# Kernel optimization log

Hardware: AMD Instinct MI355X
Metric: run time of the kernel (lower is better)

Reference implementation:

```python
import jax, jax.numpy as jnp
import numpy as np

HIDDEN_DIM = 64
MEMORY_SLOTS = 8
SEQ_LEN = 64
VOCAB_SIZE = 64
B = 524288


def setup_inputs() -> dict:
    key = jax.random.key(0)
    k1, k2, k3, k4, k5, k6 = jax.random.split(key, 6)
    seqs = jax.random.randint(k1, (B, SEQ_LEN), 0, VOCAB_SIZE + 2, dtype=jnp.int64 if jax.config.jax_enable_x64 else jnp.int32)
    query_tok = jax.random.randint(k2, (B,), 0, VOCAB_SIZE + 2, dtype=seqs.dtype)
    embed = jax.random.normal(k3, (VOCAB_SIZE + 2, HIDDEN_DIM), dtype=jnp.float32)
    # torch Linear: y = x @ W.T + b
    W1 = jax.random.normal(k4, (HIDDEN_DIM, HIDDEN_DIM * 2), dtype=jnp.float32) * (1.0 / np.sqrt(HIDDEN_DIM * 2))
    b1 = jnp.zeros((HIDDEN_DIM,), dtype=jnp.float32)
    W2 = jax.random.normal(k5, (VOCAB_SIZE, HIDDEN_DIM), dtype=jnp.float32) * (1.0 / np.sqrt(HIDDEN_DIM))
    b2 = jnp.zeros((VOCAB_SIZE,), dtype=jnp.float32)
    return {"seqs": seqs, "query_tok": query_tok, "embed": embed,
            "W1": W1, "b1": b1, "W2": W2, "b2": b2}


def reference(seqs, query_tok, embed, W1, b1, W2, b2):
    # FIFO of capacity MEMORY_SLOTS over tokens t=0..SEQ_LEN-2 keeps exactly the
    # last MEMORY_SLOTS tokens: positions [SEQ_LEN-1-MEMORY_SLOTS, SEQ_LEN-1).
    win = seqs[:, SEQ_LEN - 1 - MEMORY_SLOTS : SEQ_LEN - 1]        # [B, 8]
    mem_summary = embed[win].mean(axis=1)                          # [B, H]
    q_emb = embed[query_tok]                                       # [B, H]
    h = jnp.concatenate([q_emb, mem_summary], axis=-1)             # [B, 2H]
    h = jax.nn.relu(h @ W1.T + b1)                                 # [B, H]
    logits = h @ W2.T + b2                                         # [B, VOCAB]
    return logits
```

## Files before the change

kernel.cpp:

```cpp
#include <hip/hip_runtime.h>

#define HID 64
#define NTOK 66
#define SEQ 64
#define WIN0 55
#define NW 8
#define LDS_STRIDE 72
#define ITERS 8
#define ROWS_PER_ITER 64

typedef _Float16 half8 __attribute__((ext_vector_type(8)));
typedef unsigned short ushort8v __attribute__((ext_vector_type(8)));
typedef float float4v __attribute__((ext_vector_type(4)));

static __device__ __forceinline__ unsigned short f2h(float f) {
    _Float16 h = (_Float16)f;
    union { _Float16 h; unsigned short u; } v; v.h = h;
    return v.u;
}

__global__ void build_tables(const float* __restrict__ embed,
                             const float* __restrict__ W1,
                             const float* __restrict__ b1,
                             unsigned short* __restrict__ tbl) {
    int b = blockIdx.x;
    int tb = b & 1;
    int t  = b >> 1;
    int n  = threadIdx.x;
    float acc = tb ? 0.0f : b1[n];
    const float* er = embed + t * HID;
    const float* wr = W1 + n * (2 * HID) + tb * HID;
#pragma unroll 8
    for (int k = 0; k < HID; ++k) acc += er[k] * wr[k];
    if (tb) acc *= 0.125f;
    tbl[tb * (NTOK * HID) + t * HID + n] = f2h(acc);
}

__global__ __launch_bounds__(256, 3) void fused_forward(
    const int* __restrict__ seqs,
    const int* __restrict__ qtok,
    const float* __restrict__ W2,
    const float* __restrict__ b2,
    const unsigned short* __restrict__ tbl,
    float* __restrict__ out)
{
    __shared__ unsigned short T_lds[2 * NTOK * LDS_STRIDE];

    int tid  = threadIdx.x;
    int wv   = tid >> 6;
    int l    = tid & 63;
    int lrow = l & 15;
    int lg   = l >> 4;
    int lk8  = lg * 8;

    int row0 = blockIdx.x * (ITERS * ROWS_PER_ITER) + wv * 16 + lrow;

    int qA, qB;
    int wA[NW], wB[NW];
    half8  g[9];
    half8  a0, a1;
    float4v acc4[4];

#define LOADT(s, t_) { \
    int row_ = row0 + (t_) * ROWS_PER_ITER; \
    q##s = qtok[row_]; \
    const int* sp_ = seqs + row_ * SEQ + WIN0; \
    _Pragma("unroll") \
    for (int j = 0; j < NW; ++j) w##s[j] = sp_[j]; \
}

#define GATHER_ALL(qq, ww, k0c) { \
    g[8] = *(const half8*)(T_lds + (qq) * LDS_STRIDE + (k0c)); \
    _Pragma("unroll") \
    for (int j = 0; j < NW; ++j) \
        g[j] = *(const half8*)(T_lds + NTOK * LDS_STRIDE + (ww)[j] * LDS_STRIDE + (k0c)); \
}

#define SUM_REISSUE(aout, qq, ww, k0c) { \
    half8 s_ = g[8]; \
    g[8] = *(const half8*)(T_lds + (qq) * LDS_STRIDE + (k0c)); \
    _Pragma("unroll") \
    for (int j = 0; j < NW; ++j) { \
        s_ += g[j]; \
        g[j] = *(const half8*)(T_lds + NTOK * LDS_STRIDE + (ww)[j] * LDS_STRIDE + (k0c)); \
    } \
    half8 z_ = (half8)(_Float16)0; \
    aout = __builtin_elementwise_max(s_, z_); \
}

#define SUM_FINAL(aout) { \
    half8 s_ = g[8]; \
    _Pragma("unroll") \
    for (int j = 0; j < NW; ++j) s_ += g[j]; \
    half8 z_ = (half8)(_Float16)0; \
    aout = __builtin_elementwise_max(s_, z_); \
}

#define MFMA_K0 { \
    _Pragma("unroll") \
    for (int nt = 0; nt < 4; ++nt) \
        acc4[nt] = __builtin_amdgcn_mfma_f32_16x16x32_f16(wfrag[nt][0], a0, b2v[nt], 0, 0, 0); \
}

#define MFMA_K1_ST(t_) { \
    float* op = out + (size_t)(row0 + (t_) * ROWS_PER_ITER) * HID; \
    _Pragma("unroll") \
    for (int nt = 0; nt < 4; ++nt) { \
        acc4[nt] = __builtin_amdgcn_mfma_f32_16x16x32_f16(wfrag[nt][1], a1, acc4[nt], 0, 0, 0); \
        *(float4v*)(op + nt * 16 + lg * 4) = acc4[nt]; \
    } \
}

#define ITER_MID(C, N, t_) { \
    SUM_REISSUE(a0, q##C, w##C, 32 + lk8); \
    MFMA_K0; \
    SUM_REISSUE(a1, q##N, w##N, lk8); \
    MFMA_K1_ST(t_); \
    LOADT(C, (t_) + 2); \
}
#define ITER_NOLOAD(C, N, t_) { \
    SUM_REISSUE(a0, q##C, w##C, 32 + lk8); \
    MFMA_K0; \
    SUM_REISSUE(a1, q##N, w##N, lk8); \
    MFMA_K1_ST(t_); \
}
#define ITER_LAST(C, t_) { \
    SUM_REISSUE(a0, q##C, w##C, 32 + lk8); \
    MFMA_K0; \
    SUM_FINAL(a1); \
    MFMA_K1_ST(t_); \
}

    LOADT(A, 0);
    LOADT(B, 1);

    half8   wfrag[4][2];
    float4v b2v[4];
#pragma unroll
    for (int nt = 0; nt < 4; ++nt) {
        b2v[nt] = *(const float4v*)(b2 + nt * 16 + lg * 4);
#pragma unroll
        for (int kc = 0; kc < 2; ++kc) {
            const float* wp = W2 + (nt * 16 + lrow) * HID + kc * 32 + lk8;
            half8 f;
#pragma unroll
            for (int j = 0; j < 8; ++j) f[j] = (_Float16)wp[j];
            wfrag[nt][kc] = f;
        }
    }

    for (int i = tid; i < 2 * NTOK * (HID / 8); i += 256) {
        int tbi = i / (NTOK * 8);
        int rem = i - tbi * (NTOK * 8);
        int t   = rem >> 3;
        int kq  = (rem & 7) << 3;
        *(ushort8v*)(T_lds + tbi * (NTOK * LDS_STRIDE) + t * LDS_STRIDE + kq) =
            *(const ushort8v*)(tbl + tbi * (NTOK * HID) + t * HID + kq);
    }
    __syncthreads();

    GATHER_ALL(qA, wA, lk8);

    ITER_MID(A, B, 0);
    ITER_MID(B, A, 1);
    ITER_MID(A, B, 2);
    ITER_MID(B, A, 3);
    ITER_MID(A, B, 4);
    ITER_MID(B, A, 5);
    ITER_NOLOAD(A, B, 6);
    ITER_LAST(B, 7);

#undef LOADT
#undef GATHER_ALL
#undef SUM_REISSUE
#undef SUM_FINAL
#undef MFMA_K0
#undef MFMA_K1_ST
#undef ITER_MID
#undef ITER_NOLOAD
#undef ITER_LAST
}

extern "C" void kernel_launch(void* const* d_in, const int* in_sizes, int n_in,
                              void* d_out, int out_size, void* d_ws, size_t ws_size,
                              hipStream_t stream) {
    const int*   seqs  = (const int*)d_in[0];
    const int*   qtok  = (const int*)d_in[1];
    const float* embed = (const float*)d_in[2];
    const float* W1    = (const float*)d_in[3];
    const float* b1    = (const float*)d_in[4];
    const float* W2    = (const float*)d_in[5];
    const float* b2    = (const float*)d_in[6];
    float* out = (float*)d_out;
    unsigned short* tbl = (unsigned short*)d_ws;

    int B = in_sizes[0] / SEQ;

    build_tables<<<NTOK * 2, HID, 0, stream>>>(embed, W1, b1, tbl);

    int grid = B / (ITERS * ROWS_PER_ITER);
    fused_forward<<<grid, 256, 0, stream>>>(seqs, qtok, W2, b2, tbl, out);
}
```

Measured before the change: 48.82 us.

## Precompute pairwise window-token sums and gather from global instead of LDS

Builds a 66x66 table of pre-summed fp16 pairs of window-token projections, so each row gathers 4 pair entries plus the query entry instead of 9 entries. The gathers now read this table from global memory (L2-resident) instead of staging tables in LDS, which removes the per-block LDS fill and the barrier. The cost is an extra launch to build roughly half a megabyte of pair table and more L2 gather traffic. The old LDS path is kept as a fallback when the workspace is too small.

```diff
diff --git a/kernel.cpp b/kernel.cpp
--- a/kernel.cpp
+++ b/kernel.cpp
@@ -5,9 +5,15 @@
 #define SEQ 64
 #define WIN0 55
 #define NW 8
-#define LDS_STRIDE 72
+#define NP 4
 #define ITERS 8
 #define ROWS_PER_ITER 64
+#define LDS_STRIDE 72
+
+#define T1_OFF 0
+#define T2_OFF (NTOK * HID)
+#define TP_OFF (2 * NTOK * HID)
+#define WS_NEED_BYTES ((size_t)(2 * NTOK * HID + NTOK * NTOK * HID) * 2)
 
 typedef _Float16 half8 __attribute__((ext_vector_type(8)));
 typedef unsigned short ushort8v __attribute__((ext_vector_type(8)));
@@ -36,7 +42,160 @@
     tbl[tb * (NTOK * HID) + t * HID + n] = f2h(acc);
 }
 
-__global__ __launch_bounds__(256, 3) void fused_forward(
+__global__ void build_pairs(const unsigned short* __restrict__ tbl,
+                            unsigned short* __restrict__ ws) {
+    int idx = blockIdx.x * 64 + threadIdx.x;
+    int p = idx >> 3;
+    int c = (idx & 7) << 3;
+    if (p >= NTOK * NTOK) return;
+    int a = p / NTOK;
+    int b = p - a * NTOK;
+    half8 va = *(const half8*)(tbl + T2_OFF + a * HID + c);
+    half8 vb = *(const half8*)(tbl + T2_OFF + b * HID + c);
+    half8 s = va + vb;
+    *(half8*)(ws + TP_OFF + p * HID + c) = s;
+}
+
+__global__ __launch_bounds__(256, 3) void fused_forward_gp(
+    const int* __restrict__ seqs,
+    const int* __restrict__ qtok,
+    const float* __restrict__ W2,
+    const float* __restrict__ b2,
+    const unsigned short* __restrict__ ws,
+    float* __restrict__ out)
+{
+    int tid  = threadIdx.x;
+    int wv   = tid >> 6;
+    int l    = tid & 63;
+    int lrow = l & 15;
+    int lg   = l >> 4;
+    int lk8  = lg * 8;
+
+    int row0 = blockIdx.x * (ITERS * ROWS_PER_ITER) + wv * 16 + lrow;
+
+    const unsigned short* t1p = ws + T1_OFF;
+    const unsigned short* tpp = ws + TP_OFF;
+
+    int qA, qB;
+    int pA[NP], pB[NP];
+    half8 gP[NP + 1], gQ[NP + 1];
+    half8 a0, a1;
+    float4v acc4[4];
+
+#define LOADT(s, t_) { \
+    int row_ = row0 + (t_) * ROWS_PER_ITER; \
+    q##s = qtok[row_]; \
+    const int* sp_ = seqs + row_ * SEQ + WIN0; \
+    int w0_=sp_[0], w1_=sp_[1], w2_=sp_[2], w3_=sp_[3]; \
+    int w4_=sp_[4], w5_=sp_[5], w6_=sp_[6], w7_=sp_[7]; \
+    p##s[0] = w0_ * NTOK + w1_;  p##s[1] = w2_ * NTOK + w3_; \
+    p##s[2] = w4_ * NTOK + w5_;  p##s[3] = w6_ * NTOK + w7_; \
+}
+
+#define GATHER(g, qq, pp, koff) { \
+    (g)[NP] = *(const half8*)(t1p + (qq) * HID + (koff)); \
+    _Pragma("unroll") \
+    for (int j = 0; j < NP; ++j) \
+        (g)[j] = *(const half8*)(tpp + (pp)[j] * HID + (koff)); \
+}
+
+#define SUM_REISSUE(aout, g, qq, pp, koff) { \
+    half8 s_ = (g)[NP]; \
+    (g)[NP] = *(const half8*)(t1p + (qq) * HID + (koff)); \
+    _Pragma("unroll") \
+    for (int j = 0; j < NP; ++j) { \
+        s_ += (g)[j]; \
+        (g)[j] = *(const half8*)(tpp + (pp)[j] * HID + (koff)); \
+    } \
+    half8 z_ = (half8)(_Float16)0; \
+    aout = __builtin_elementwise_max(s_, z_); \
+}
+
+#define SUM_FINAL(aout, g) { \
+    half8 s_ = (g)[NP]; \
+    _Pragma("unroll") \
+    for (int j = 0; j < NP; ++j) s_ += (g)[j]; \
+    half8 z_ = (half8)(_Float16)0; \
+    aout = __builtin_elementwise_max(s_, z_); \
+}
+
+#define MFMA_K0 { \
+    _Pragma("unroll") \
+    for (int nt = 0; nt < 4; ++nt) \
+        acc4[nt] = __builtin_amdgcn_mfma_f32_16x16x32_f16(wfrag[nt][0], a0, b2v[nt], 0, 0, 0); \
+}
+
+#define MFMA_K1_ST(t_) { \
+    float* op = out + (size_t)(row0 + (t_) * ROWS_PER_ITER) * HID; \
+    _Pragma("unroll") \
+    for (int nt = 0; nt < 4; ++nt) { \
+        acc4[nt] = __builtin_amdgcn_mfma_f32_16x16x32_f16(wfrag[nt][1], a1, acc4[nt], 0, 0, 0); \
+        *(float4v*)(op + nt * 16 + lg * 4) = acc4[nt]; \
+    } \
+}
+
+#define ITER_MID(C, N, t_) { \
+    SUM_REISSUE(a0, gP, q##N, p##N, lk8); \
+    MFMA_K0; \
+    SUM_REISSUE(a1, gQ, q##N, p##N, 32 + lk8); \
+    MFMA_K1_ST(t_); \
+    LOADT(C, (t_) + 2); \
+}
+#define ITER_NOLOAD(C, N, t_) { \
+    SUM_REISSUE(a0, gP, q##N, p##N, lk8); \
+    MFMA_K0; \
+    SUM_REISSUE(a1, gQ, q##N, p##N, 32 + lk8); \
+    MFMA_K1_ST(t_); \
+}
+#define ITER_LAST(C, t_) { \
+    SUM_FINAL(a0, gP); \
+    MFMA_K0; \
+    SUM_FINAL(a1, gQ); \
+    MFMA_K1_ST(t_); \
+}
+
+    LOADT(A, 0);
+    LOADT(B, 1);
+
+    half8   wfrag[4][2];
+    float4v b2v[4];
+#pragma unroll
+    for (int nt = 0; nt < 4; ++nt) {
+        b2v[nt] = *(const float4v*)(b2 + nt * 16 + lg * 4);
+#pragma unroll
+        for (int kc = 0; kc < 2; ++kc) {
+            const float* wp = W2 + (nt * 16 + lrow) * HID + kc * 32 + lk8;
+            half8 f;
+#pragma unroll
+            for (int j = 0; j < 8; ++j) f[j] = (_Float16)wp[j];
+            wfrag[nt][kc] = f;
+        }
+    }
+
+    GATHER(gP, qA, pA, lk8);
+    GATHER(gQ, qA, pA, 32 + lk8);
+
+    ITER_MID(A, B, 0);
+    ITER_MID(B, A, 1);
+    ITER_MID(A, B, 2);
+    ITER_MID(B, A, 3);
+    ITER_MID(A, B, 4);
+    ITER_MID(B, A, 5);
+    ITER_NOLOAD(A, B, 6);
+    ITER_LAST(B, 7);
+
+#undef LOADT
+#undef GATHER
+#undef SUM_REISSUE
+#undef SUM_FINAL
+#undef MFMA_K0
+#undef MFMA_K1_ST
+#undef ITER_MID
+#undef ITER_NOLOAD
+#undef ITER_LAST
+}
+
+__global__ __launch_bounds__(256, 3) void fused_forward_lds(
     const int* __restrict__ seqs,
     const int* __restrict__ qtok,
     const float* __restrict__ W2,
@@ -68,14 +227,12 @@
     _Pragma("unroll") \
     for (int j = 0; j < NW; ++j) w##s[j] = sp_[j]; \
 }
-
 #define GATHER_ALL(qq, ww, k0c) { \
     g[8] = *(const half8*)(T_lds + (qq) * LDS_STRIDE + (k0c)); \
     _Pragma("unroll") \
     for (int j = 0; j < NW; ++j) \
         g[j] = *(const half8*)(T_lds + NTOK * LDS_STRIDE + (ww)[j] * LDS_STRIDE + (k0c)); \
 }
-
 #define SUM_REISSUE(aout, qq, ww, k0c) { \
     half8 s_ = g[8]; \
     g[8] = *(const half8*)(T_lds + (qq) * LDS_STRIDE + (k0c)); \
@@ -87,7 +244,6 @@
     half8 z_ = (half8)(_Float16)0; \
     aout = __builtin_elementwise_max(s_, z_); \
 }
-
 #define SUM_FINAL(aout) { \
     half8 s_ = g[8]; \
     _Pragma("unroll") \
@@ -95,13 +251,11 @@
     half8 z_ = (half8)(_Float16)0; \
     aout = __builtin_elementwise_max(s_, z_); \
 }
-
 #define MFMA_K0 { \
     _Pragma("unroll") \
     for (int nt = 0; nt < 4; ++nt) \
         acc4[nt] = __builtin_amdgcn_mfma_f32_16x16x32_f16(wfrag[nt][0], a0, b2v[nt], 0, 0, 0); \
 }
-
 #define MFMA_K1_ST(t_) { \
     float* op = out + (size_t)(row0 + (t_) * ROWS_PER_ITER) * HID; \
     _Pragma("unroll") \
@@ -110,7 +264,6 @@
         *(float4v*)(op + nt * 16 + lg * 4) = acc4[nt]; \
     } \
 }
-
 #define ITER_MID(C, N, t_) { \
     SUM_REISSUE(a0, q##C, w##C, 32 + lk8); \
     MFMA_K0; \
@@ -195,9 +348,15 @@
     unsigned short* tbl = (unsigned short*)d_ws;
 
     int B = in_sizes[0] / SEQ;
+    int grid = B / (ITERS * ROWS_PER_ITER);
 
     build_tables<<<NTOK * 2, HID, 0, stream>>>(embed, W1, b1, tbl);
 
-    int grid = B / (ITERS * ROWS_PER_ITER);
-    fused_forward<<<grid, 256, 0, stream>>>(seqs, qtok, W2, b2, tbl, out);
-}
+    if (ws_size >= WS_NEED_BYTES) {
+        int pgrid = (NTOK * NTOK * 8 + 63) / 64;
+        build_pairs<<<pgrid, 64, 0, stream>>>(tbl, tbl);
+        fused_forward_gp<<<grid, 256, 0, stream>>>(seqs, qtok, W2, b2, tbl, out);
+    } else {
+        fused_forward_lds<<<grid, 256, 0, stream>>>(seqs, qtok, W2, b2, tbl, out);
+    }
+}
```

After: 73.39 us. +50.3%, slower.
